# Optimization experiments

Hardware: AMD Instinct MI355X
Metric: run time of the kernel (lower is better)

The kernel has to match this reference:

```python
import jax, jax.numpy as jnp
import numpy as np


def _min_dist_mean(a, b):
    # a: (B, N, 3), b: (B, M, 3). Euclidean cdist via ||a||^2 + ||b||^2 - 2 a.b
    a2 = jnp.sum(a * a, axis=-1)                      # (B, N)
    b2 = jnp.sum(b * b, axis=-1)                      # (B, M)
    ab = jnp.einsum('bnd,bmd->bnm', a, b)             # (B, N, M)
    d2 = a2[:, :, None] + b2[:, None, :] - 2.0 * ab   # (B, N, M)
    d = jnp.sqrt(jnp.maximum(d2, 1e-12))              # matches torch.cdist p=2
    return jnp.mean(jnp.min(d, axis=-1))


def setup_inputs() -> dict:
    key = jax.random.key(0)
    k1, k2 = jax.random.split(key)
    template = jax.random.normal(k1, (4, 8192, 3), dtype=jnp.float32)
    source = jax.random.normal(k2, (4, 8192, 3), dtype=jnp.float32)
    return {"template": template, "source": source}


def reference(template, source):
    loss_a_to_b = _min_dist_mean(template, source)
    loss_b_to_a = _min_dist_mean(source, template)
    return loss_a_to_b + loss_b_to_a
```

## Files before the change

kernel.cpp:

```cpp
#include <hip/hip_runtime.h>

#define BATCH 4
#define NPTS 8192
#define CLOUD_PTS (BATCH * NPTS)
#define TOTAL_ROWS (2 * BATCH * NPTS)

typedef __attribute__((ext_vector_type(8))) short bf16x8;
typedef __attribute__((ext_vector_type(16))) float f32x16;

__device__ __forceinline__ unsigned fkey(float f) {
    unsigned u = __float_as_uint(f);
    return (u & 0x80000000u) ? ~u : (u | 0x80000000u);
}
__device__ __forceinline__ float funkey(unsigned k) {
    return (k & 0x80000000u) ? __uint_as_float(k ^ 0x80000000u) : __uint_as_float(~k);
}
__device__ __forceinline__ unsigned short bf16rn(float f) {
    unsigned u = __float_as_uint(f);
    return (unsigned short)((u + 0x7FFFu + ((u >> 16) & 1u)) >> 16);
}
__device__ __forceinline__ float bf2f(unsigned short h) {
    return __uint_as_float(((unsigned)h) << 16);
}

__global__ __launch_bounds__(256) void prep_kernel(
    const float* __restrict__ tpl, const float* __restrict__ src,
    unsigned short* __restrict__ featA, unsigned short* __restrict__ featB,
    unsigned int* __restrict__ keys)
{
    const int gid = blockIdx.x * 256 + threadIdx.x;
    keys[gid] = 0xFFFFFFFFu;

    const int cloud = gid >> 15;
    const int idx = gid & (CLOUD_PTS - 1);
    const float* p = (cloud ? src : tpl) + (size_t)idx * 3;
    const float x = p[0], y = p[1], z = p[2];
    const float n2 = fmaf(x, x, fmaf(y, y, z * z));
    const unsigned short n2h = bf16rn(n2);
    const unsigned short n2l = bf16rn(n2 - bf2f(n2h));
    const unsigned short ONE = 0x3F80;

    const unsigned short hx = bf16rn(x), hy = bf16rn(y), hz = bf16rn(z);
    const unsigned short lx = bf16rn(x - bf2f(hx));
    const unsigned short ly = bf16rn(y - bf2f(hy));
    const unsigned short lz = bf16rn(z - bf2f(hz));
    const float mx = -2.0f * x, my = -2.0f * y, mz = -2.0f * z;
    const unsigned short ahx = bf16rn(mx), ahy = bf16rn(my), ahz = bf16rn(mz);
    const unsigned short alx = bf16rn(mx - bf2f(ahx));
    const unsigned short aly = bf16rn(my - bf2f(ahy));
    const unsigned short alz = bf16rn(mz - bf2f(ahz));

    __attribute__((aligned(16))) unsigned short fA[16] = {
        ahx, ahy, ahz, alx, aly, alz, ahx, ahy, ahz, n2h, n2l, ONE, ONE, 0, 0, 0};
    __attribute__((aligned(16))) unsigned short fB[16] = {
        hx, hy, hz, hx, hy, hz, lx, ly, lz, ONE, ONE, n2h, n2l, 0, 0, 0};

    unsigned short* oA = featA + ((size_t)cloud * CLOUD_PTS + idx) * 16;
    unsigned short* oB = featB + ((size_t)cloud * CLOUD_PTS + idx) * 16;
    *(float4*)&oA[0] = *(float4*)&fA[0];
    *(float4*)&oA[8] = *(float4*)&fA[8];
    *(float4*)&oB[0] = *(float4*)&fB[0];
    *(float4*)&oB[8] = *(float4*)&fB[8];
}

__global__ __launch_bounds__(256, 4) void chamfer_mfma_kernel(
    const unsigned short* __restrict__ featA,
    const unsigned short* __restrict__ featB,
    unsigned int* __restrict__ keys)
{
    __shared__ __align__(16) unsigned char smem[4 * 64 * 33 * 4];
    unsigned short* sB = (unsigned short*)smem;
    float* sEp = (float*)smem;

    const int aSlab = blockIdx.x;
    const int bChnk = blockIdx.y;
    const int dir   = blockIdx.z & 1;
    const int batch = blockIdx.z >> 1;

    const int t    = threadIdx.x;
    const int w    = t >> 6;
    const int lane = t & 63;
    const int col  = lane & 31;
    const int half = lane >> 5;

    const unsigned short* Af =
        featA + ((size_t)(dir * CLOUD_PTS + batch * NPTS + aSlab * 256)) * 16;
    const unsigned short* Bf =
        featB + ((size_t)((1 - dir) * CLOUD_PTS + batch * NPTS + bChnk * 2048)) * 16;

    bf16x8 afr[2];
#pragma unroll
    for (int a = 0; a < 2; ++a)
        afr[a] = *(const bf16x8*)(Af + ((size_t)(w * 64 + a * 32 + col)) * 16 + half * 8);

    float vmin[2][16];
#pragma unroll
    for (int a = 0; a < 2; ++a)
#pragma unroll
        for (int r = 0; r < 16; ++r) vmin[a][r] = 3.0e38f;

    const f32x16 ZERO = (f32x16)(0.0f);

#pragma unroll 1
    for (int phase = 0; phase < 2; ++phase) {
        const float4* gB = (const float4*)(Bf + (size_t)phase * 1024 * 16);
#pragma unroll
        for (int i = 0; i < 8; ++i) {
            const int c = t + i * 256;
            const int pt = c >> 1, h = c & 1;
            *(float4*)&sB[((size_t)(h * 1024 + pt)) * 8] = gB[c];
        }
        __syncthreads();

        const unsigned short* sBh = &sB[(size_t)(half * 1024) * 8];
#pragma unroll 8
        for (int bt = 0; bt < 32; ++bt) {
            const bf16x8 bfr = *(const bf16x8*)&sBh[((size_t)(bt * 32 + col)) * 8];
#pragma unroll
            for (int a = 0; a < 2; ++a) {
                const f32x16 d = __builtin_amdgcn_mfma_f32_32x32x16_bf16(afr[a], bfr, ZERO, 0, 0, 0);
#pragma unroll
                for (int r = 0; r < 16; ++r) vmin[a][r] = fminf(vmin[a][r], d[r]);
            }
        }
        __syncthreads();
    }

    float* ep = sEp + (size_t)w * (64 * 33);
#pragma unroll
    for (int a = 0; a < 2; ++a)
#pragma unroll
        for (int r = 0; r < 16; ++r)
            ep[lane * 33 + a * 16 + r] = vmin[a][r];
    __syncthreads();

    const int a_   = lane >> 5;
    const int rit  = lane & 31;
    const int hsrc = (rit >> 2) & 1;
    const int r_   = (rit & 3) | (((rit >> 3) & 3) << 2);
    const float* src0 = ep + (size_t)(hsrc * 32) * 33 + (a_ * 16 + r_);

    float m = 3.0e38f;
#pragma unroll
    for (int c = 0; c < 32; ++c)
        m = fminf(m, src0[c * 33]);

    unsigned int* rowKey = keys + dir * CLOUD_PTS + batch * NPTS;
    atomicMin(&rowKey[aSlab * 256 + w * 64 + lane], fkey(m));
}

__global__ __launch_bounds__(256) void reduce_rows_kernel(
    const unsigned int* __restrict__ minkey, float* __restrict__ blockSums)
{
    const int gid = blockIdx.x * 256 + threadIdx.x;
    const float v = funkey(minkey[gid]);
    float d = sqrtf(fmaxf(v, 1e-12f));
#pragma unroll
    for (int off = 32; off; off >>= 1) d += __shfl_down(d, off);
    __shared__ float wsum[4];
    const int wave = threadIdx.x >> 6, lane = threadIdx.x & 63;
    if (lane == 0) wsum[wave] = d;
    __syncthreads();
    if (threadIdx.x == 0)
        blockSums[blockIdx.x] = (wsum[0] + wsum[1]) + (wsum[2] + wsum[3]);
}

__global__ __launch_bounds__(256) void final_kernel(
    const float* __restrict__ blockSums, float* __restrict__ out)
{
    float d = blockSums[threadIdx.x];
#pragma unroll
    for (int off = 32; off; off >>= 1) d += __shfl_down(d, off);
    __shared__ float wsum[4];
    const int wave = threadIdx.x >> 6, lane = threadIdx.x & 63;
    if (lane == 0) wsum[wave] = d;
    __syncthreads();
    if (threadIdx.x == 0) {
        const float total = (wsum[0] + wsum[1]) + (wsum[2] + wsum[3]);
        out[0] = total / (float)(BATCH * NPTS);
    }
}

extern "C" void kernel_launch(void* const* d_in, const int* in_sizes, int n_in,
                              void* d_out, int out_size, void* d_ws, size_t ws_size,
                              hipStream_t stream) {
    const float* tpl = (const float*)d_in[0];
    const float* src = (const float*)d_in[1];
    float* out = (float*)d_out;

    unsigned short* featA = (unsigned short*)d_ws;
    unsigned short* featB = featA + (size_t)2 * CLOUD_PTS * 16;
    unsigned int* keys    = (unsigned int*)((char*)d_ws + 4u * 1024 * 1024);
    float* blockSums      = (float*)(keys + TOTAL_ROWS);

    prep_kernel<<<TOTAL_ROWS / 256, 256, 0, stream>>>(tpl, src, featA, featB, keys);

    dim3 grid(NPTS / 256, NPTS / 2048, 2 * BATCH);
    chamfer_mfma_kernel<<<grid, 256, 0, stream>>>(featA, featB, keys);

    reduce_rows_kernel<<<TOTAL_ROWS / 256, 256, 0, stream>>>(keys, blockSums);
    final_kernel<<<1, 256, 0, stream>>>(blockSums, out);
}
```

Measured before the change: 31.09 us.

## Fuse feature prep into MFMA kernel and replace atomics with per-chunk partials

Removes the separate prep kernel: the main kernel now reads raw xyz floats and builds the split-bf16 A and B features in registers and shared memory itself. Row minima are no longer combined with atomicMin on sortable keys. Each B-chunk writes its own partial minimum, and the reduce kernel takes the min over the chunks. This drops one launch, the feature round-trip through global memory and the atomics, at the cost of redundant bf16 conversion work in every block and a larger partials buffer.

```diff
diff --git a/kernel.cpp b/kernel.cpp
--- a/kernel.cpp
+++ b/kernel.cpp
@@ -4,17 +4,11 @@
 #define NPTS 8192
 #define CLOUD_PTS (BATCH * NPTS)
 #define TOTAL_ROWS (2 * BATCH * NPTS)
+#define NCHUNK 4
 
 typedef __attribute__((ext_vector_type(8))) short bf16x8;
 typedef __attribute__((ext_vector_type(16))) float f32x16;
 
-__device__ __forceinline__ unsigned fkey(float f) {
-    unsigned u = __float_as_uint(f);
-    return (u & 0x80000000u) ? ~u : (u | 0x80000000u);
-}
-__device__ __forceinline__ float funkey(unsigned k) {
-    return (k & 0x80000000u) ? __uint_as_float(k ^ 0x80000000u) : __uint_as_float(~k);
-}
 __device__ __forceinline__ unsigned short bf16rn(float f) {
     unsigned u = __float_as_uint(f);
     return (unsigned short)((u + 0x7FFFu + ((u >> 16) & 1u)) >> 16);
@@ -23,50 +17,9 @@
     return __uint_as_float(((unsigned)h) << 16);
 }
 
-__global__ __launch_bounds__(256) void prep_kernel(
+__global__ __launch_bounds__(256, 4) void chamfer_main_kernel(
     const float* __restrict__ tpl, const float* __restrict__ src,
-    unsigned short* __restrict__ featA, unsigned short* __restrict__ featB,
-    unsigned int* __restrict__ keys)
-{
-    const int gid = blockIdx.x * 256 + threadIdx.x;
-    keys[gid] = 0xFFFFFFFFu;
-
-    const int cloud = gid >> 15;
-    const int idx = gid & (CLOUD_PTS - 1);
-    const float* p = (cloud ? src : tpl) + (size_t)idx * 3;
-    const float x = p[0], y = p[1], z = p[2];
-    const float n2 = fmaf(x, x, fmaf(y, y, z * z));
-    const unsigned short n2h = bf16rn(n2);
-    const unsigned short n2l = bf16rn(n2 - bf2f(n2h));
-    const unsigned short ONE = 0x3F80;
-
-    const unsigned short hx = bf16rn(x), hy = bf16rn(y), hz = bf16rn(z);
-    const unsigned short lx = bf16rn(x - bf2f(hx));
-    const unsigned short ly = bf16rn(y - bf2f(hy));
-    const unsigned short lz = bf16rn(z - bf2f(hz));
-    const float mx = -2.0f * x, my = -2.0f * y, mz = -2.0f * z;
-    const unsigned short ahx = bf16rn(mx), ahy = bf16rn(my), ahz = bf16rn(mz);
-    const unsigned short alx = bf16rn(mx - bf2f(ahx));
-    const unsigned short aly = bf16rn(my - bf2f(ahy));
-    const unsigned short alz = bf16rn(mz - bf2f(ahz));
-
-    __attribute__((aligned(16))) unsigned short fA[16] = {
-        ahx, ahy, ahz, alx, aly, alz, ahx, ahy, ahz, n2h, n2l, ONE, ONE, 0, 0, 0};
-    __attribute__((aligned(16))) unsigned short fB[16] = {
-        hx, hy, hz, hx, hy, hz, lx, ly, lz, ONE, ONE, n2h, n2l, 0, 0, 0};
-
-    unsigned short* oA = featA + ((size_t)cloud * CLOUD_PTS + idx) * 16;
-    unsigned short* oB = featB + ((size_t)cloud * CLOUD_PTS + idx) * 16;
-    *(float4*)&oA[0] = *(float4*)&fA[0];
-    *(float4*)&oA[8] = *(float4*)&fA[8];
-    *(float4*)&oB[0] = *(float4*)&fB[0];
-    *(float4*)&oB[8] = *(float4*)&fB[8];
-}
-
-__global__ __launch_bounds__(256, 4) void chamfer_mfma_kernel(
-    const unsigned short* __restrict__ featA,
-    const unsigned short* __restrict__ featB,
-    unsigned int* __restrict__ keys)
+    float* __restrict__ partials)
 {
     __shared__ __align__(16) unsigned char smem[4 * 64 * 33 * 4];
     unsigned short* sB = (unsigned short*)smem;
@@ -83,15 +36,29 @@
     const int col  = lane & 31;
     const int half = lane >> 5;
 
-    const unsigned short* Af =
-        featA + ((size_t)(dir * CLOUD_PTS + batch * NPTS + aSlab * 256)) * 16;
-    const unsigned short* Bf =
-        featB + ((size_t)((1 - dir) * CLOUD_PTS + batch * NPTS + bChnk * 2048)) * 16;
+    const float* Acloud = (dir ? src : tpl) + (size_t)batch * NPTS * 3;
+    const float* Bcloud = (dir ? tpl : src) + (size_t)batch * NPTS * 3;
+
+    const short ONE = (short)0x3F80;
 
     bf16x8 afr[2];
 #pragma unroll
-    for (int a = 0; a < 2; ++a)
-        afr[a] = *(const bf16x8*)(Af + ((size_t)(w * 64 + a * 32 + col)) * 16 + half * 8);
+    for (int a = 0; a < 2; ++a) {
+        const float* p = Acloud + (size_t)(aSlab * 256 + w * 64 + a * 32 + col) * 3;
+        const float x = p[0], y = p[1], z = p[2];
+        const float n2 = fmaf(x, x, fmaf(y, y, z * z));
+        const unsigned short n2h = bf16rn(n2);
+        const unsigned short n2l = bf16rn(n2 - bf2f(n2h));
+        const float mx = -2.0f * x, my = -2.0f * y, mz = -2.0f * z;
+        const unsigned short ahx = bf16rn(mx), ahy = bf16rn(my), ahz = bf16rn(mz);
+        const unsigned short alx = bf16rn(mx - bf2f(ahx));
+        const unsigned short aly = bf16rn(my - bf2f(ahy));
+        const unsigned short alz = bf16rn(mz - bf2f(ahz));
+        const bf16x8 f0 = {(short)ahx, (short)ahy, (short)ahz, (short)alx,
+                           (short)aly, (short)alz, (short)ahx, (short)ahy};
+        const bf16x8 f1 = {(short)ahz, (short)n2h, (short)n2l, ONE, ONE, 0, 0, 0};
+        afr[a] = half ? f1 : f0;
+    }
 
     float vmin[2][16];
 #pragma unroll
@@ -103,12 +70,32 @@
 
 #pragma unroll 1
     for (int phase = 0; phase < 2; ++phase) {
-        const float4* gB = (const float4*)(Bf + (size_t)phase * 1024 * 16);
+        {
+            const float4* g4 =
+                (const float4*)(Bcloud + (size_t)(bChnk * 2048 + phase * 1024) * 3);
+            const float4 v0 = g4[t * 3 + 0];
+            const float4 v1 = g4[t * 3 + 1];
+            const float4 v2 = g4[t * 3 + 2];
+            const float px[4] = {v0.x, v0.w, v1.z, v2.y};
+            const float py[4] = {v0.y, v1.x, v1.w, v2.z};
+            const float pz[4] = {v0.z, v1.y, v2.x, v2.w};
 #pragma unroll
-        for (int i = 0; i < 8; ++i) {
-            const int c = t + i * 256;
-            const int pt = c >> 1, h = c & 1;
-            *(float4*)&sB[((size_t)(h * 1024 + pt)) * 8] = gB[c];
+            for (int i = 0; i < 4; ++i) {
+                const int pt = t * 4 + i;
+                const float x = px[i], y = py[i], z = pz[i];
+                const float n2 = fmaf(x, x, fmaf(y, y, z * z));
+                const unsigned short n2h = bf16rn(n2);
+                const unsigned short n2l = bf16rn(n2 - bf2f(n2h));
+                const unsigned short hx = bf16rn(x), hy = bf16rn(y), hz = bf16rn(z);
+                const unsigned short lx = bf16rn(x - bf2f(hx));
+                const unsigned short ly = bf16rn(y - bf2f(hy));
+                const unsigned short lz = bf16rn(z - bf2f(hz));
+                const bf16x8 h0 = {(short)hx, (short)hy, (short)hz, (short)hx,
+                                   (short)hy, (short)hz, (short)lx, (short)ly};
+                const bf16x8 h1 = {(short)lz, ONE, ONE, (short)n2h, (short)n2l, 0, 0, 0};
+                *(bf16x8*)&sB[((size_t)(0 * 1024 + pt)) * 8] = h0;
+                *(bf16x8*)&sB[((size_t)(1 * 1024 + pt)) * 8] = h1;
+            }
         }
         __syncthreads();
 
@@ -145,16 +132,19 @@
     for (int c = 0; c < 32; ++c)
         m = fminf(m, src0[c * 33]);
 
-    unsigned int* rowKey = keys + dir * CLOUD_PTS + batch * NPTS;
-    atomicMin(&rowKey[aSlab * 256 + w * 64 + lane], fkey(m));
+    const int row = dir * CLOUD_PTS + batch * NPTS + aSlab * 256 + w * 64 + lane;
+    partials[(size_t)bChnk * TOTAL_ROWS + row] = m;
 }
 
 __global__ __launch_bounds__(256) void reduce_rows_kernel(
-    const unsigned int* __restrict__ minkey, float* __restrict__ blockSums)
+    const float* __restrict__ partials, float* __restrict__ blockSums)
 {
     const int gid = blockIdx.x * 256 + threadIdx.x;
-    const float v = funkey(minkey[gid]);
-    float d = sqrtf(fmaxf(v, 1e-12f));
+    float m = partials[gid];
+#pragma unroll
+    for (int c = 1; c < NCHUNK; ++c)
+        m = fminf(m, partials[(size_t)c * TOTAL_ROWS + gid]);
+    float d = sqrtf(fmaxf(m, 1e-12f));
 #pragma unroll
     for (int off = 32; off; off >>= 1) d += __shfl_down(d, off);
     __shared__ float wsum[4];
@@ -188,16 +178,12 @@
     const float* src = (const float*)d_in[1];
     float* out = (float*)d_out;
 
-    unsigned short* featA = (unsigned short*)d_ws;
-    unsigned short* featB = featA + (size_t)2 * CLOUD_PTS * 16;
-    unsigned int* keys    = (unsigned int*)((char*)d_ws + 4u * 1024 * 1024);
-    float* blockSums      = (float*)(keys + TOTAL_ROWS);
+    float* partials  = (float*)d_ws;
+    float* blockSums = partials + (size_t)NCHUNK * TOTAL_ROWS;
 
-    prep_kernel<<<TOTAL_ROWS / 256, 256, 0, stream>>>(tpl, src, featA, featB, keys);
+    dim3 grid(NPTS / 256, NCHUNK, 2 * BATCH);
+    chamfer_main_kernel<<<grid, 256, 0, stream>>>(tpl, src, partials);
 
-    dim3 grid(NPTS / 256, NPTS / 2048, 2 * BATCH);
-    chamfer_mfma_kernel<<<grid, 256, 0, stream>>>(featA, featB, keys);
-
-    reduce_rows_kernel<<<TOTAL_ROWS / 256, 256, 0, stream>>>(keys, blockSums);
+    reduce_rows_kernel<<<TOTAL_ROWS / 256, 256, 0, stream>>>(partials, blockSums);
     final_kernel<<<1, 256, 0, stream>>>(blockSums, out);
 }
```

Result: slower. 33.95 us (+9.2%).

## Replace atomicMin row keys with per-chunk partials and fuse final reduction

Applied to the files above, without the earlier changes.

The chamfer kernel now writes each row's partial minimum for its B-chunk to a separate plane instead of doing atomicMin on an ordered-int key. The reduce kernel takes the min over the four chunk planes, then uses a last-block counter pattern to compute the final mean, so the separate final kernel launch goes away. This removes the global atomics and one launch, at the cost of four times as many partial writes and reads plus a threadfence and atomic counter.

```diff
diff --git a/kernel.cpp b/kernel.cpp
--- a/kernel.cpp
+++ b/kernel.cpp
@@ -4,17 +4,11 @@
 #define NPTS 8192
 #define CLOUD_PTS (BATCH * NPTS)
 #define TOTAL_ROWS (2 * BATCH * NPTS)
+#define NCHUNK 4
 
 typedef __attribute__((ext_vector_type(8))) short bf16x8;
 typedef __attribute__((ext_vector_type(16))) float f32x16;
 
-__device__ __forceinline__ unsigned fkey(float f) {
-    unsigned u = __float_as_uint(f);
-    return (u & 0x80000000u) ? ~u : (u | 0x80000000u);
-}
-__device__ __forceinline__ float funkey(unsigned k) {
-    return (k & 0x80000000u) ? __uint_as_float(k ^ 0x80000000u) : __uint_as_float(~k);
-}
 __device__ __forceinline__ unsigned short bf16rn(float f) {
     unsigned u = __float_as_uint(f);
     return (unsigned short)((u + 0x7FFFu + ((u >> 16) & 1u)) >> 16);
@@ -26,10 +20,10 @@
 __global__ __launch_bounds__(256) void prep_kernel(
     const float* __restrict__ tpl, const float* __restrict__ src,
     unsigned short* __restrict__ featA, unsigned short* __restrict__ featB,
-    unsigned int* __restrict__ keys)
+    unsigned int* __restrict__ counter)
 {
     const int gid = blockIdx.x * 256 + threadIdx.x;
-    keys[gid] = 0xFFFFFFFFu;
+    if (gid == 0) *counter = 0;
 
     const int cloud = gid >> 15;
     const int idx = gid & (CLOUD_PTS - 1);
@@ -66,7 +60,7 @@
 __global__ __launch_bounds__(256, 4) void chamfer_mfma_kernel(
     const unsigned short* __restrict__ featA,
     const unsigned short* __restrict__ featB,
-    unsigned int* __restrict__ keys)
+    float* __restrict__ partials)
 {
     __shared__ __align__(16) unsigned char smem[4 * 64 * 33 * 4];
     unsigned short* sB = (unsigned short*)smem;
@@ -145,39 +139,45 @@
     for (int c = 0; c < 32; ++c)
         m = fminf(m, src0[c * 33]);
 
-    unsigned int* rowKey = keys + dir * CLOUD_PTS + batch * NPTS;
-    atomicMin(&rowKey[aSlab * 256 + w * 64 + lane], fkey(m));
-}
-
-__global__ __launch_bounds__(256) void reduce_rows_kernel(
-    const unsigned int* __restrict__ minkey, float* __restrict__ blockSums)
+    const int row = dir * CLOUD_PTS + batch * NPTS + aSlab * 256 + w * 64 + lane;
+    partials[(size_t)bChnk * TOTAL_ROWS + row] = m;
+}
+
+__global__ __launch_bounds__(256) void reduce_final_kernel(
+    const float* __restrict__ partials, float* __restrict__ blockSums,
+    unsigned int* __restrict__ counter, float* __restrict__ out)
 {
     const int gid = blockIdx.x * 256 + threadIdx.x;
-    const float v = funkey(minkey[gid]);
-    float d = sqrtf(fmaxf(v, 1e-12f));
+    float m = partials[gid];
+#pragma unroll
+    for (int c = 1; c < NCHUNK; ++c)
+        m = fminf(m, partials[(size_t)c * TOTAL_ROWS + gid]);
+    float d = sqrtf(fmaxf(m, 1e-12f));
 #pragma unroll
     for (int off = 32; off; off >>= 1) d += __shfl_down(d, off);
     __shared__ float wsum[4];
-    const int wave = threadIdx.x >> 6, lane = threadIdx.x & 63;
-    if (lane == 0) wsum[wave] = d;
-    __syncthreads();
-    if (threadIdx.x == 0)
-        blockSums[blockIdx.x] = (wsum[0] + wsum[1]) + (wsum[2] + wsum[3]);
-}
-
-__global__ __launch_bounds__(256) void final_kernel(
-    const float* __restrict__ blockSums, float* __restrict__ out)
-{
-    float d = blockSums[threadIdx.x];
-#pragma unroll
-    for (int off = 32; off; off >>= 1) d += __shfl_down(d, off);
-    __shared__ float wsum[4];
+    __shared__ int isLast;
     const int wave = threadIdx.x >> 6, lane = threadIdx.x & 63;
     if (lane == 0) wsum[wave] = d;
     __syncthreads();
     if (threadIdx.x == 0) {
-        const float total = (wsum[0] + wsum[1]) + (wsum[2] + wsum[3]);
-        out[0] = total / (float)(BATCH * NPTS);
+        blockSums[blockIdx.x] = (wsum[0] + wsum[1]) + (wsum[2] + wsum[3]);
+        __threadfence();
+        const unsigned old = atomicAdd(counter, 1u);
+        isLast = (old == (TOTAL_ROWS / 256) - 1) ? 1 : 0;
+    }
+    __syncthreads();
+    if (isLast) {
+        __threadfence();
+        float s = blockSums[threadIdx.x];
+#pragma unroll
+        for (int off = 32; off; off >>= 1) s += __shfl_down(s, off);
+        if (lane == 0) wsum[wave] = s;
+        __syncthreads();
+        if (threadIdx.x == 0) {
+            const float total = (wsum[0] + wsum[1]) + (wsum[2] + wsum[3]);
+            out[0] = total / (float)(BATCH * NPTS);
+        }
     }
 }
 
@@ -189,15 +189,15 @@
     float* out = (float*)d_out;
 
     unsigned short* featA = (unsigned short*)d_ws;
-    unsigned short* featB = featA + (size_t)2 * CLOUD_PTS * 16;
-    unsigned int* keys    = (unsigned int*)((char*)d_ws + 4u * 1024 * 1024);
-    float* blockSums      = (float*)(keys + TOTAL_ROWS);
-
-    prep_kernel<<<TOTAL_ROWS / 256, 256, 0, stream>>>(tpl, src, featA, featB, keys);
-
-    dim3 grid(NPTS / 256, NPTS / 2048, 2 * BATCH);
-    chamfer_mfma_kernel<<<grid, 256, 0, stream>>>(featA, featB, keys);
-
-    reduce_rows_kernel<<<TOTAL_ROWS / 256, 256, 0, stream>>>(keys, blockSums);
-    final_kernel<<<1, 256, 0, stream>>>(blockSums, out);
-}
+    unsigned short* featB = featA + (size_t)CLOUD_PTS * 2 * 16;
+    float* partials  = (float*)((char*)d_ws + 4u * 1024 * 1024);
+    float* blockSums = partials + (size_t)NCHUNK * TOTAL_ROWS;
+    unsigned int* counter = (unsigned int*)(blockSums + 256);
+
+    prep_kernel<<<TOTAL_ROWS / 256, 256, 0, stream>>>(tpl, src, featA, featB, counter);
+
+    dim3 grid(NPTS / 256, NCHUNK, 2 * BATCH);
+    chamfer_mfma_kernel<<<grid, 256, 0, stream>>>(featA, featB, partials);
+
+    reduce_final_kernel<<<TOTAL_ROWS / 256, 256, 0, stream>>>(partials, blockSums, counter, out);
+}
```

Result: slower. 35.75 us (+15.0%).
